# Optimization experiments

Measured on AMD Instinct MI355X. Metric: run time of the kernel, lower is better.

## Reference

```python
import jax, jax.numpy as jnp
import numpy as np

N_NODES = 100000
N_EDGES = 1600000
D_IN = 256
D_OUT = 256


def setup_inputs() -> dict:
    key = jax.random.key(0)
    k1, k2, k3, k4, k5 = jax.random.split(key, 5)
    feat = jax.random.normal(k1, (N_NODES, D_IN), dtype=jnp.float32)
    src = jax.random.randint(k2, (N_EDGES,), 0, N_NODES, dtype=jnp.int32)
    dst = jax.random.randint(k3, (N_EDGES,), 0, N_NODES, dtype=jnp.int32)
    # xavier_uniform with gain for relu (sqrt(2)), as in reset_parameters
    gain = float(np.sqrt(2.0))
    limit = gain * float(np.sqrt(6.0 / (D_IN + D_OUT)))
    w_neigh = jax.random.uniform(k4, (D_OUT, D_IN), minval=-limit, maxval=limit, dtype=jnp.float32)
    w_self = jax.random.uniform(k5, (D_OUT, D_IN), minval=-limit, maxval=limit, dtype=jnp.float32)
    b_self = jnp.zeros((D_OUT,), dtype=jnp.float32)
    return {"feat": feat, "src": src, "dst": dst,
            "w_neigh": w_neigh, "w_self": w_self, "b_self": b_self}


def reference(feat, src, dst, w_neigh, w_self, b_self):
    # SAGEConv, aggregator_type='mean', feat_drop=0, no edge_weight.
    # lin_before_mp = (in_feats > out_feats) = False -> aggregate raw feats first.
    n = feat.shape[0]
    # gather messages at edges and segment-sum into dst nodes
    summed = jax.ops.segment_sum(feat[src], dst, num_segments=n)  # [N, D_in]
    deg = jax.ops.segment_sum(jnp.ones_like(dst, dtype=feat.dtype), dst, num_segments=n)
    h_neigh_raw = summed / jnp.maximum(deg, 1.0)[:, None]  # mean; 0 for isolated nodes
    h_neigh = h_neigh_raw @ w_neigh.T                       # fc_neigh (no bias)
    rst = feat @ w_self.T + b_self + h_neigh                # fc_self(h_self) + h_neigh
    return rst
```

## Files before the change

### kernel.cpp

```cpp
#include <hip/hip_runtime.h>
#include <cstddef>

#define N_NODES 100000
#define N_EDGES 1600000
#define D 256

typedef short          s16x8 __attribute__((ext_vector_type(8)));
typedef unsigned short u16x8 __attribute__((ext_vector_type(8)));
typedef float          f32x4 __attribute__((ext_vector_type(4)));
typedef float          f32x8 __attribute__((ext_vector_type(8)));

__device__ __forceinline__ unsigned short f2bf(float f) {
    unsigned int u = __float_as_uint(f);
    unsigned int r = (u + 0x7fffu + ((u >> 16) & 1u)) >> 16;
    return (unsigned short)r;
}
__device__ __forceinline__ float bf2f(unsigned short u) {
    return __uint_as_float(((unsigned int)u) << 16);
}

#define WS_COUNTS 0
#define WS_ROWPTR (N_NODES)
#define WS_COL    (2 * N_NODES + 16)
#define WS_PART   (WS_COL + N_EDGES)
#define WB_BYTE   ((size_t)(WS_PART + 128) * 4)
#define FB_BYTE   (WB_BYTE + 2 * 65536 * 2)
#define FB_SZ     ((size_t)N_NODES * D * 2)
#define FQ_BYTE   FB_BYTE
#define FQ_SZ     ((size_t)N_NODES * D)
#define HB3_BYTE  (FQ_BYTE + FQ_SZ)
#define NEED_XL3  (HB3_BYTE + FB_SZ)
#define NEED_LARGE (FB_BYTE + FB_SZ)
#define NEED_MID  (FB_BYTE)

#define FBLOCKS (N_NODES * D / 8 / 256)
#define SCAN_NB ((N_NODES + 1023) / 1024)
#define GEMMBLKS ((N_NODES + 63) / 64)
#define NSLICE 8
#define SLICE_N (N_NODES / NSLICE)
#define ECHUNK 2048
#define ECHUNKS ((N_EDGES + ECHUNK - 1) / ECHUNK)
#define SLICED_NB (ECHUNKS * NSLICE)

__global__ __launch_bounds__(256) void cvt_u8_kernel(
    const float* __restrict__ feat, const float* __restrict__ w_self,
    const float* __restrict__ w_neigh,
    unsigned char* __restrict__ fq, unsigned short* __restrict__ wb)
{
    const int b = blockIdx.x;
    if (b < FBLOCKS) {
        const int i = b * 256 + threadIdx.x;
        const f32x8 v = ((const f32x8*)feat)[i];
        unsigned int p0 = 0, p1 = 0;
#pragma unroll
        for (int k = 0; k < 4; ++k) {
            int q = (int)rintf(fminf(fmaxf(v[k] * 16.0f, -127.0f), 127.0f)) + 128;
            p0 |= ((unsigned int)q) << (8 * k);
        }
#pragma unroll
        for (int k = 0; k < 4; ++k) {
            int q = (int)rintf(fminf(fmaxf(v[4 + k] * 16.0f, -127.0f), 127.0f)) + 128;
            p1 |= ((unsigned int)q) << (8 * k);
        }
        uint2 o; o.x = p0; o.y = p1;
        *(uint2*)(fq + (size_t)i * 8) = o;
    } else {
        const int i = (b - FBLOCKS) * 256 + threadIdx.x;
        const bool isself = (i < 16384);
        const float* srcp = isself ? w_self : w_neigh;
        const int j = (isself ? i : i - 16384) * 4;
        const float4 v = *(const float4*)(srcp + j);
        ushort4 o;
        o.x = f2bf(v.x); o.y = f2bf(v.y); o.z = f2bf(v.z); o.w = f2bf(v.w);
        ((ushort4*)wb)[i] = o;
    }
}

__global__ __launch_bounds__(256) void cvt_bf16_kernel(
    const float* __restrict__ feat, const float* __restrict__ w_self,
    const float* __restrict__ w_neigh,
    unsigned short* __restrict__ fb, unsigned short* __restrict__ wb)
{
    const int b = blockIdx.x;
    if (b < FBLOCKS) {
        const int i = b * 256 + threadIdx.x;
        const f32x8 v = ((const f32x8*)feat)[i];
        ushort4 a, c;
        a.x = f2bf(v[0]); a.y = f2bf(v[1]); a.z = f2bf(v[2]); a.w = f2bf(v[3]);
        c.x = f2bf(v[4]); c.y = f2bf(v[5]); c.z = f2bf(v[6]); c.w = f2bf(v[7]);
        ((ushort4*)fb)[i * 2 + 0] = a;
        ((ushort4*)fb)[i * 2 + 1] = c;
    } else {
        const int i = (b - FBLOCKS) * 256 + threadIdx.x;
        const bool isself = (i < 16384);
        const float* srcp = isself ? w_self : w_neigh;
        const int j = (isself ? i : i - 16384) * 4;
        const float4 v = *(const float4*)(srcp + j);
        ushort4 o;
        o.x = f2bf(v.x); o.y = f2bf(v.y); o.z = f2bf(v.z); o.w = f2bf(v.w);
        ((ushort4*)wb)[i] = o;
    }
}

__global__ __launch_bounds__(256) void wcvt_kernel(
    const float* __restrict__ w_self, const float* __restrict__ w_neigh,
    unsigned short* __restrict__ wb)
{
    const int i = blockIdx.x * 256 + threadIdx.x;
    const bool isself = (i < 16384);
    const float* srcp = isself ? w_self : w_neigh;
    const int j = (isself ? i : i - 16384) * 4;
    const float4 v = *(const float4*)(srcp + j);
    ushort4 o;
    o.x = f2bf(v.x); o.y = f2bf(v.y); o.z = f2bf(v.z); o.w = f2bf(v.w);
    ((ushort4*)wb)[i] = o;
}

__global__ __launch_bounds__(256) void hist_sliced_kernel(
    const int* __restrict__ dst, int* __restrict__ counts)
{
    const int slice = blockIdx.x & (NSLICE - 1);
    const int chunk = blockIdx.x >> 3;
    const int lo = slice * SLICE_N, hi = lo + SLICE_N;
    const int e0 = chunk * ECHUNK + threadIdx.x * 8;
    if (e0 >= N_EDGES) return;
    if (e0 + 8 <= N_EDGES) {
        const int4 d0 = *(const int4*)(dst + e0);
        const int4 d1 = *(const int4*)(dst + e0 + 4);
        const int dv[8] = {d0.x, d0.y, d0.z, d0.w, d1.x, d1.y, d1.z, d1.w};
#pragma unroll
        for (int k = 0; k < 8; ++k)
            if (dv[k] >= lo && dv[k] < hi) atomicAdd(&counts[dv[k]], 1);
    } else {
        for (int e = e0; e < N_EDGES; ++e) {
            const int d = dst[e];
            if (d >= lo && d < hi) atomicAdd(&counts[d], 1);
        }
    }
}

__global__ __launch_bounds__(1024) void scan_block_kernel(
    const int* __restrict__ counts, int* __restrict__ row_ptr,
    int* __restrict__ partials)
{
    __shared__ int wsum[16];
    const int t = threadIdx.x, b = blockIdx.x, i = b * 1024 + t;
    const int lane = t & 63, w = t >> 6;
    int x = (i < N_NODES) ? counts[i] : 0;
#pragma unroll
    for (int off = 1; off < 64; off <<= 1) {
        int y = __shfl_up(x, off, 64);
        if (lane >= off) x += y;
    }
    if (lane == 63) wsum[w] = x;
    __syncthreads();
    if (w == 0) {
        int s = (lane < 16) ? wsum[lane] : 0;
#pragma unroll
        for (int off = 1; off < 16; off <<= 1) {
            int y = __shfl_up(s, off, 64);
            if (lane >= off) s += y;
        }
        if (lane < 16) wsum[lane] = s;
    }
    __syncthreads();
    const int incl = x + (w > 0 ? wsum[w - 1] : 0);
    if (i < N_NODES) row_ptr[i + 1] = incl;
    if (t == 1023) partials[b] = incl;
}

__global__ __launch_bounds__(1024) void scan_add2_kernel(
    const int* __restrict__ partials, int* __restrict__ row_ptr)
{
    __shared__ int sp[SCAN_NB];
    const int t = threadIdx.x, b = blockIdx.x;
    if (t < SCAN_NB) sp[t] = partials[t];
    __syncthreads();
    int off = 0;
    for (int j = 0; j < b; ++j) off += sp[j];
    const int i = b * 1024 + t;
    if (i < N_NODES) row_ptr[i + 1] += off;
    if (b == 0 && t == 0) row_ptr[0] = 0;
}

__global__ __launch_bounds__(256) void fill_sliced_kernel(
    const int* __restrict__ src, const int* __restrict__ dst,
    const int* __restrict__ row_ptr, int* __restrict__ counts,
    int* __restrict__ col)
{
    const int slice = blockIdx.x & (NSLICE - 1);
    const int chunk = blockIdx.x >> 3;
    const int lo = slice * SLICE_N, hi = lo + SLICE_N;
    const int e0 = chunk * ECHUNK + threadIdx.x * 8;
    if (e0 >= N_EDGES) return;
    if (e0 + 8 <= N_EDGES) {
        const int4 d0 = *(const int4*)(dst + e0);
        const int4 d1 = *(const int4*)(dst + e0 + 4);
        const int4 s0 = *(const int4*)(src + e0);
        const int4 s1 = *(const int4*)(src + e0 + 4);
        const int dv[8] = {d0.x, d0.y, d0.z, d0.w, d1.x, d1.y, d1.z, d1.w};
        const int sv[8] = {s0.x, s0.y, s0.z, s0.w, s1.x, s1.y, s1.z, s1.w};
#pragma unroll
        for (int k = 0; k < 8; ++k) {
            const int d = dv[k];
            if (d >= lo && d < hi) {
                const int pos = atomicSub(&counts[d], 1) - 1;
                col[row_ptr[d] + pos] = sv[k];
            }
        }
    } else {
        for (int e = e0; e < N_EDGES; ++e) {
            const int d = dst[e];
            if (d >= lo && d < hi) {
                const int pos = atomicSub(&counts[d], 1) - 1;
                col[row_ptr[d] + pos] = src[e];
            }
        }
    }
}

__global__ __launch_bounds__(256) void aggregate4_kernel(
    const unsigned char* __restrict__ fq,
    const int* __restrict__ row_ptr, const int* __restrict__ col,
    unsigned short* __restrict__ hb)
{
    const int node = (blockIdx.x * blockDim.x + threadIdx.x) >> 6;
    const int lane = threadIdx.x & 63;
    if (node >= N_NODES) return;
    const int beg = row_ptr[node], end = row_ptr[node + 1];
    const int quarter = lane >> 4;
    const int chunk = lane & 15;

    unsigned int aE[4] = {0,0,0,0}, aO[4] = {0,0,0,0};
    unsigned int bE[4] = {0,0,0,0}, bO[4] = {0,0,0,0};
    const unsigned char* base = fq + chunk * 16;

    int j = beg + quarter;
    for (; j + 4 < end; j += 8) {
        const int s0 = col[j];
        const int s1 = col[j + 4];
        const uint4 u = *(const uint4*)(base + (size_t)s0 * D);
        const uint4 v = *(const uint4*)(base + (size_t)s1 * D);
        aE[0] += u.x & 0x00FF00FFu;  aO[0] += (u.x >> 8) & 0x00FF00FFu;
        aE[1] += u.y & 0x00FF00FFu;  aO[1] += (u.y >> 8) & 0x00FF00FFu;
        aE[2] += u.z & 0x00FF00FFu;  aO[2] += (u.z >> 8) & 0x00FF00FFu;
        aE[3] += u.w & 0x00FF00FFu;  aO[3] += (u.w >> 8) & 0x00FF00FFu;
        bE[0] += v.x & 0x00FF00FFu;  bO[0] += (v.x >> 8) & 0x00FF00FFu;
        bE[1] += v.y & 0x00FF00FFu;  bO[1] += (v.y >> 8) & 0x00FF00FFu;
        bE[2] += v.z & 0x00FF00FFu;  bO[2] += (v.z >> 8) & 0x00FF00FFu;
        bE[3] += v.w & 0x00FF00FFu;  bO[3] += (v.w >> 8) & 0x00FF00FFu;
    }
    for (; j < end; j += 4) {
        const int s0 = col[j];
        const uint4 u = *(const uint4*)(base + (size_t)s0 * D);
        aE[0] += u.x & 0x00FF00FFu;  aO[0] += (u.x >> 8) & 0x00FF00FFu;
        aE[1] += u.y & 0x00FF00FFu;  aO[1] += (u.y >> 8) & 0x00FF00FFu;
        aE[2] += u.z & 0x00FF00FFu;  aO[2] += (u.z >> 8) & 0x00FF00FFu;
        aE[3] += u.w & 0x00FF00FFu;  aO[3] += (u.w >> 8) & 0x00FF00FFu;
    }

#pragma unroll
    for (int d = 0; d < 4; ++d) {
        unsigned int e = aE[d] + bE[d];
        unsigned int o = aO[d] + bO[d];
        e += __shfl_xor((int)e, 16, 64);
        e += __shfl_xor((int)e, 32, 64);
        o += __shfl_xor((int)o, 16, 64);
        o += __shfl_xor((int)o, 32, 64);
        aE[d] = e; aO[d] = o;
    }

    if (quarter == 0) {
        const int deg = end - beg;
        const float inv = 1.0f / (16.0f * fmaxf((float)deg, 1.0f));
        const float bias = 128.0f * (float)deg;
        u16x8 o0, o1;
#pragma unroll
        for (int d = 0; d < 4; ++d) {
            const float e0 = ((float)(aE[d] & 0xFFFFu) - bias) * inv;
            const float e2 = ((float)(aE[d] >> 16)     - bias) * inv;
            const float e1 = ((float)(aO[d] & 0xFFFFu) - bias) * inv;
            const float e3 = ((float)(aO[d] >> 16)     - bias) * inv;
            if (d < 2) {
                o0[d * 4 + 0] = f2bf(e0); o0[d * 4 + 1] = f2bf(e1);
                o0[d * 4 + 2] = f2bf(e2); o0[d * 4 + 3] = f2bf(e3);
            } else {
                o1[(d - 2) * 4 + 0] = f2bf(e0); o1[(d - 2) * 4 + 1] = f2bf(e1);
                o1[(d - 2) * 4 + 2] = f2bf(e2); o1[(d - 2) * 4 + 3] = f2bf(e3);
            }
        }
        unsigned short* op = hb + (size_t)node * D + chunk * 16;
        *(u16x8*)op = o0;
        *(u16x8*)(op + 8) = o1;
    }
}

__global__ __launch_bounds__(256) void gemm_v5_kernel(
    const float* __restrict__ feat,
    const unsigned short* __restrict__ hb,
    const unsigned short* __restrict__ wb,
    const float* __restrict__ b_self,
    float* __restrict__ outp)
{
    __shared__ unsigned short As[2][64 * 64];

    const int t    = threadIdx.x;
    const int lane = t & 63;
    const int w    = t >> 6;
    const int row0 = blockIdx.x * 64;
    const int c0   = w * 64;
    const int nl   = lane & 15;
    const int kg   = lane >> 4;

    const int tr = t >> 2;
    const int tq = t & 3;
    int grow = row0 + tr; if (grow > N_NODES - 1) grow = N_NODES - 1;
    const size_t gf = (size_t)grow * D;

    int wsw[2];
#pragma unroll
    for (int c = 0; c < 2; ++c) {
        const int cs = tq * 16 + c * 8;
        wsw[c] = tr * 64 + (cs ^ ((tr & 7) << 3));
    }
    int rsw[4][2];
#pragma unroll
    for (int m = 0; m < 4; ++m) {
        const int r = m * 16 + nl;
#pragma unroll
        for (int kk = 0; kk < 2; ++kk) {
            const int cs = kg * 8 + kk * 32;
            rsw[m][kk] = r * 64 + (cs ^ ((r & 7) << 3));
        }
    }

    f32x4 acc[4][4];
#pragma unroll
    for (int m = 0; m < 4; ++m)
#pragma unroll
        for (int n = 0; n < 4; ++n) acc[m][n] = (f32x4){0.f, 0.f, 0.f, 0.f};

    f32x8 fA0, fA1, fB0, fB1;
    u16x8 hA0, hA1, hB0, hB1;

#define LOADSET(F0, F1, H0, H1, S) do {                                       \
        if ((S) < 4) {                                                        \
            F0 = *(const f32x8*)(feat + gf + (S) * 64 + tq * 16);             \
            F1 = *(const f32x8*)(feat + gf + (S) * 64 + tq * 16 + 8);         \
        } else {                                                              \
            H0 = *(const u16x8*)(hb + gf + ((S) & 3) * 64 + tq * 16);         \
            H1 = *(const u16x8*)(hb + gf + ((S) & 3) * 64 + tq * 16 + 8);     \
        }                                                                     \
    } while (0)

#define WRITESET(F0, F1, H0, H1, S) do {                                      \
        u16x8 w0_, w1_;                                                       \
        if ((S) < 4) {                                                        \
            _Pragma("unroll") for (int i_ = 0; i_ < 8; ++i_) {                \
                w0_[i_] = f2bf(F0[i_]); w1_[i_] = f2bf(F1[i_]);               \
            }                                                                 \
        } else { w0_ = H0; w1_ = H1; }                                        \
        *(u16x8*)&As[(S) & 1][wsw[0]] = w0_;                                  \
        *(u16x8*)&As[(S) & 1][wsw[1]] = w1_;                                  \
    } while (0)

    LOADSET(fA0, fA1, hA0, hA1, 0);
    LOADSET(fB0, fB1, hB0, hB1, 1);

#pragma unroll
    for (int s = 0; s < 8; ++s) {
        if ((s & 1) == 0) WRITESET(fA0, fA1, hA0, hA1, s);
        else              WRITESET(fB0, fB1, hB0, hB1, s);
        __syncthreads();
        if (s + 2 < 8) {
            if ((s & 1) == 0) LOADSET(fA0, fA1, hA0, hA1, s + 2);
            else              LOADSET(fB0, fB1, hB0, hB1, s + 2);
        }
        const int hsel = (s < 4) ? 0 : 65536;
        const int kbase = (s & 3) * 64;
#pragma unroll
        for (int kk = 0; kk < 2; ++kk) {
            s16x8 a[4], b[4];
#pragma unroll
            for (int m = 0; m < 4; ++m)
                a[m] = *(const s16x8*)&As[s & 1][rsw[m][kk]];
#pragma unroll
            for (int n = 0; n < 4; ++n)
                b[n] = *(const s16x8*)(wb + hsel
                        + (size_t)(c0 + n * 16 + nl) * 256 + kbase + kk * 32 + kg * 8);
#pragma unroll
            for (int m = 0; m < 4; ++m)
#pragma unroll
                for (int n = 0; n < 4; ++n)
                    acc[m][n] = __builtin_amdgcn_mfma_f32_16x16x32_bf16(
                        a[m], b[n], acc[m][n], 0, 0, 0);
        }
    }
#undef LOADSET
#undef WRITESET

#pragma unroll
    for (int n = 0; n < 4; ++n) {
        const float bias = b_self[c0 + n * 16 + nl];
#pragma unroll
        for (int m = 0; m < 4; ++m) {
            const int rbase = row0 + m * 16 + kg * 4;
#pragma unroll
            for (int r = 0; r < 4; ++r) {
                const int row = rbase + r;
                if (row < N_NODES)
                    outp[(size_t)row * D + c0 + n * 16 + nl] = acc[m][n][r] + bias;
            }
        }
    }
}

__global__ __launch_bounds__(256) void aggregate2f_kernel(
    const unsigned short* __restrict__ featb,
    const int* __restrict__ row_ptr, const int* __restrict__ col,
    float* __restrict__ outf)
{
    const int node = (blockIdx.x * blockDim.x + threadIdx.x) >> 6;
    const int lane = threadIdx.x & 63;
    if (node >= N_NODES) return;
    const int beg = row_ptr[node], end = row_ptr[node + 1];
    const int half = lane >> 5;
    const int chunk = lane & 31;

    float a0[8] = {0,0,0,0,0,0,0,0};
    float a1[8] = {0,0,0,0,0,0,0,0};
    float a2[8] = {0,0,0,0,0,0,0,0};
    float a3[8] = {0,0,0,0,0,0,0,0};
    const unsigned short* fbp = featb + chunk * 8;

    int j = beg + half;
    for (; j + 6 < end; j += 8) {
        const int s0 = col[j], s1 = col[j + 2], s2 = col[j + 4], s3 = col[j + 6];
        const u16x8 u0 = *(const u16x8*)(fbp + (size_t)s0 * D);
        const u16x8 u1 = *(const u16x8*)(fbp + (size_t)s1 * D);
        const u16x8 u2 = *(const u16x8*)(fbp + (size_t)s2 * D);
        const u16x8 u3 = *(const u16x8*)(fbp + (size_t)s3 * D);
#pragma unroll
        for (int i = 0; i < 8; ++i) a0[i] += bf2f(u0[i]);
#pragma unroll
        for (int i = 0; i < 8; ++i) a1[i] += bf2f(u1[i]);
#pragma unroll
        for (int i = 0; i < 8; ++i) a2[i] += bf2f(u2[i]);
#pragma unroll
        for (int i = 0; i < 8; ++i) a3[i] += bf2f(u3[i]);
    }
    for (; j < end; j += 2) {
        const int s0 = col[j];
        const u16x8 u0 = *(const u16x8*)(fbp + (size_t)s0 * D);
#pragma unroll
        for (int i = 0; i < 8; ++i) a0[i] += bf2f(u0[i]);
    }

    const float invd = 1.0f / fmaxf((float)(end - beg), 1.0f);
    float tv[8];
#pragma unroll
    for (int i = 0; i < 8; ++i) {
        float v = (a0[i] + a1[i]) + (a2[i] + a3[i]);
        v += __shfl_xor(v, 32, 64);
        tv[i] = v * invd;
    }
    float4 o;
    o.x = tv[half * 4 + 0]; o.y = tv[half * 4 + 1];
    o.z = tv[half * 4 + 2]; o.w = tv[half * 4 + 3];
    *(float4*)(outf + (size_t)node * D + chunk * 8 + half * 4) = o;
}

__global__ __launch_bounds__(256) void aggregate_f32_kernel(
    const float* __restrict__ feat, const int* __restrict__ row_ptr,
    const int* __restrict__ col, float* __restrict__ outf)
{
    const int node = (blockIdx.x * blockDim.x + threadIdx.x) >> 6;
    const int lane = threadIdx.x & 63;
    if (node >= N_NODES) return;
    const int beg = row_ptr[node], end = row_ptr[node + 1];

    float4 a0 = make_float4(0.f, 0.f, 0.f, 0.f);
    float4 a1 = make_float4(0.f, 0.f, 0.f, 0.f);
    float4 a2 = make_float4(0.f, 0.f, 0.f, 0.f);
    float4 a3 = make_float4(0.f, 0.f, 0.f, 0.f);

#define ACC(acc, s)                                                          \
    do {                                                                     \
        const float4 v = ((const float4*)(feat + (size_t)(s) * D))[lane];    \
        acc.x += v.x; acc.y += v.y; acc.z += v.z; acc.w += v.w;              \
    } while (0)

    int j = beg;
    for (; j + 3 < end; j += 4) {
        const int s0 = col[j], s1 = col[j + 1], s2 = col[j + 2], s3 = col[j + 3];
        ACC(a0, s0); ACC(a1, s1); ACC(a2, s2); ACC(a3, s3);
    }
    for (; j < end; ++j) { const int s0 = col[j]; ACC(a0, s0); }
#undef ACC

    const float invd = 1.0f / fmaxf((float)(end - beg), 1.0f);
    float4 r;
    r.x = ((a0.x + a1.x) + (a2.x + a3.x)) * invd;
    r.y = ((a0.y + a1.y) + (a2.y + a3.y)) * invd;
    r.z = ((a0.z + a1.z) + (a2.z + a3.z)) * invd;
    r.w = ((a0.w + a1.w) + (a2.w + a3.w)) * invd;
    ((float4*)(outf + (size_t)node * D))[lane] = r;
}

__global__ __launch_bounds__(256) void gemm_mfma64_f32h_kernel(
    const float* __restrict__ feat,
    const unsigned short* __restrict__ wb,
    const float* __restrict__ b_self,
    const float* h32, float* outp)
{
    const int lane = threadIdx.x & 63;
    const int wslice = threadIdx.x >> 6;
    const int row0 = blockIdx.x * 64;
    const int c0 = wslice * 64;
    const int nl = lane & 15;
    const int kg = lane >> 4;

    f32x4 acc[4][4];
#pragma unroll
    for (int m = 0; m < 4; ++m)
#pragma unroll
        for (int n = 0; n < 4; ++n) acc[m][n] = (f32x4){0.f, 0.f, 0.f, 0.f};

    size_t aoff[4];
#pragma unroll
    for (int m = 0; m < 4; ++m) {
        int r = row0 + m * 16 + nl;
        if (r > N_NODES - 1) r = N_NODES - 1;
        aoff[m] = (size_t)r * D + kg * 8;
    }

#pragma unroll
    for (int hf = 0; hf < 2; ++hf) {
        const unsigned short* wh = wb + hf * 65536 + (size_t)(c0 + nl) * 256 + kg * 8;
#pragma unroll
        for (int kk = 0; kk < 8; ++kk) {
            const int kb = kk * 32;
            s16x8 afrag[4];
#pragma unroll
            for (int m = 0; m < 4; ++m) {
                const float* ap = hf == 0 ? (const float*)feat : h32;
                const f32x8 av = *(const f32x8*)(ap + aoff[m] + kb);
#pragma unroll
                for (int i = 0; i < 8; ++i) afrag[m][i] = (short)f2bf(av[i]);
            }
            s16x8 bfrag[4];
#pragma unroll
            for (int n = 0; n < 4; ++n)
                bfrag[n] = *(const s16x8*)(wh + n * 4096 + kb);
#pragma unroll
            for (int m = 0; m < 4; ++m)
#pragma unroll
                for (int n = 0; n < 4; ++n)
                    acc[m][n] = __builtin_amdgcn_mfma_f32_16x16x32_bf16(
                        afrag[m], bfrag[n], acc[m][n], 0, 0, 0);
        }
    }

    __syncthreads();

#pragma unroll
    for (int n = 0; n < 4; ++n) {
        const float bias = b_self[c0 + n * 16 + nl];
#pragma unroll
        for (int m = 0; m < 4; ++m) {
            const int rbase = row0 + m * 16 + kg * 4;
#pragma unroll
            for (int r = 0; r < 4; ++r) {
                const int row = rbase + r;
                if (row < N_NODES)
                    outp[(size_t)row * D + c0 + n * 16 + nl] = acc[m][n][r] + bias;
            }
        }
    }
}

__global__ __launch_bounds__(256) void scatter_kernel(
    const float* __restrict__ feat, const int* __restrict__ src,
    const int* __restrict__ dst, float* __restrict__ S, float* __restrict__ deg)
{
    const int gtid = blockIdx.x * blockDim.x + threadIdx.x;
    const int wave = gtid >> 6;
    const int lane = gtid & 63;
    const int nwaves = (gridDim.x * blockDim.x) >> 6;
    for (int e = wave; e < N_EDGES; e += nwaves) {
        const int s = src[e];
        const int d = dst[e];
        if (lane == 0) unsafeAtomicAdd(&deg[d], 1.0f);
        const float4 v = ((const float4*)(feat + (size_t)s * D))[lane];
        float* o = S + (size_t)d * D + lane * 4;
        unsafeAtomicAdd(o + 0, v.x);
        unsafeAtomicAdd(o + 1, v.y);
        unsafeAtomicAdd(o + 2, v.z);
        unsafeAtomicAdd(o + 3, v.w);
    }
}

#define BM 64
#define BK 16

__global__ __launch_bounds__(256) void fused_gemm_f32(
    const float* __restrict__ feat, const float* __restrict__ w_neigh,
    const float* __restrict__ w_self, const float* __restrict__ b_self,
    const float* __restrict__ deg, float* out)
{
    __shared__ float At[BK][BM + 4];
    __shared__ float Bt[BK][256];

    const int tid = threadIdx.x;
    const int i0 = blockIdx.x * BM;
    const int trow = tid >> 4;
    const int tcol = tid & 15;
    const int m_load = tid >> 2;
    const int kq = tid & 3;

    const int arow = i0 + m_load;
    const bool arow_ok = arow < N_NODES;
    float invd = 1.0f;
    if (arow_ok) invd = 1.0f / fmaxf(deg[arow], 1.0f);

    float acc[4][16];
#pragma unroll
    for (int r = 0; r < 4; ++r)
#pragma unroll
        for (int c = 0; c < 16; ++c) acc[r][c] = 0.0f;

    for (int kc = 0; kc < (2 * D) / BK; ++kc) {
        const int kb = kc * BK;
        const bool self_part = (kb < D);
        const int kbase = self_part ? kb : (kb - D);

        float4 va = make_float4(0.f, 0.f, 0.f, 0.f);
        if (arow_ok) {
            const float* ap = self_part ? feat : out;
            va = *(const float4*)(ap + (size_t)arow * D + kbase + kq * 4);
            if (!self_part) { va.x *= invd; va.y *= invd; va.z *= invd; va.w *= invd; }
        }
        const float* W = self_part ? w_self : w_neigh;
        const float4* wp = (const float4*)(W + (size_t)tid * D + kbase);
        const float4 w0 = wp[0], w1 = wp[1], w2 = wp[2], w3 = wp[3];

        __syncthreads();
        At[kq * 4 + 0][m_load] = va.x;
        At[kq * 4 + 1][m_load] = va.y;
        At[kq * 4 + 2][m_load] = va.z;
        At[kq * 4 + 3][m_load] = va.w;
        Bt[ 0][tid] = w0.x; Bt[ 1][tid] = w0.y; Bt[ 2][tid] = w0.z; Bt[ 3][tid] = w0.w;
        Bt[ 4][tid] = w1.x; Bt[ 5][tid] = w1.y; Bt[ 6][tid] = w1.z; Bt[ 7][tid] = w1.w;
        Bt[ 8][tid] = w2.x; Bt[ 9][tid] = w2.y; Bt[10][tid] = w2.z; Bt[11][tid] = w2.w;
        Bt[12][tid] = w3.x; Bt[13][tid] = w3.y; Bt[14][tid] = w3.z; Bt[15][tid] = w3.w;
        __syncthreads();

#pragma unroll
        for (int k = 0; k < BK; ++k) {
            const float4 a = *(const float4*)&At[k][trow * 4];
            float4 b[4];
#pragma unroll
            for (int g = 0; g < 4; ++g)
                b[g] = *(const float4*)&Bt[k][g * 64 + tcol * 4];
            const float av[4] = {a.x, a.y, a.z, a.w};
#pragma unroll
            for (int r = 0; r < 4; ++r)
#pragma unroll
                for (int g = 0; g < 4; ++g) {
                    acc[r][g * 4 + 0] = fmaf(av[r], b[g].x, acc[r][g * 4 + 0]);
                    acc[r][g * 4 + 1] = fmaf(av[r], b[g].y, acc[r][g * 4 + 1]);
                    acc[r][g * 4 + 2] = fmaf(av[r], b[g].z, acc[r][g * 4 + 2]);
                    acc[r][g * 4 + 3] = fmaf(av[r], b[g].w, acc[r][g * 4 + 3]);
                }
        }
    }

    float4 bias[4];
#pragma unroll
    for (int g = 0; g < 4; ++g)
        bias[g] = *(const float4*)&b_self[g * 64 + tcol * 4];

#pragma unroll
    for (int r = 0; r < 4; ++r) {
        const int row = i0 + trow * 4 + r;
        if (row < N_NODES) {
            float* op = out + (size_t)row * D;
#pragma unroll
            for (int g = 0; g < 4; ++g) {
                float4 v;
                v.x = acc[r][g * 4 + 0] + bias[g].x;
                v.y = acc[r][g * 4 + 1] + bias[g].y;
                v.z = acc[r][g * 4 + 2] + bias[g].z;
                v.w = acc[r][g * 4 + 3] + bias[g].w;
                *(float4*)(op + g * 64 + tcol * 4) = v;
            }
        }
    }
}

extern "C" void kernel_launch(void* const* d_in, const int* in_sizes, int n_in,
                              void* d_out, int out_size, void* d_ws, size_t ws_size,
                              hipStream_t stream) {
    const float* feat    = (const float*)d_in[0];
    const int*   src     = (const int*)d_in[1];
    const int*   dst     = (const int*)d_in[2];
    const float* w_neigh = (const float*)d_in[3];
    const float* w_self  = (const float*)d_in[4];
    const float* b_self  = (const float*)d_in[5];
    float* out = (float*)d_out;

    const int ablocks = (N_NODES * 64 + 255) / 256;

    if (ws_size >= NEED_MID) {
        int* wsI     = (int*)d_ws;
        int* counts  = wsI + WS_COUNTS;
        int* row_ptr = wsI + WS_ROWPTR;
        int* col     = wsI + WS_COL;
        int* part    = wsI + WS_PART;
        unsigned short* wb = (unsigned short*)((char*)d_ws + WB_BYTE);
        unsigned short* fb = (unsigned short*)((char*)d_ws + FB_BYTE);
        unsigned char*  fq = (unsigned char*)((char*)d_ws + FQ_BYTE);
        unsigned short* hb = (unsigned short*)((char*)d_ws + HB3_BYTE);

        hipMemsetAsync(counts, 0, N_NODES * sizeof(int), stream);
        if (ws_size >= NEED_XL3)
            cvt_u8_kernel<<<FBLOCKS + 128, 256, 0, stream>>>(
                feat, w_self, w_neigh, fq, wb);
        else if (ws_size >= NEED_LARGE)
            cvt_bf16_kernel<<<FBLOCKS + 128, 256, 0, stream>>>(
                feat, w_self, w_neigh, fb, wb);
        else
            wcvt_kernel<<<128, 256, 0, stream>>>(w_self, w_neigh, wb);

        hist_sliced_kernel<<<SLICED_NB, 256, 0, stream>>>(dst, counts);
        scan_block_kernel<<<SCAN_NB, 1024, 0, stream>>>(counts, row_ptr, part);
        scan_add2_kernel<<<SCAN_NB, 1024, 0, stream>>>(part, row_ptr);
        fill_sliced_kernel<<<SLICED_NB, 256, 0, stream>>>(
            src, dst, row_ptr, counts, col);

        if (ws_size >= NEED_XL3) {
            aggregate4_kernel<<<ablocks, 256, 0, stream>>>(fq, row_ptr, col, hb);
            gemm_v5_kernel<<<GEMMBLKS, 256, 0, stream>>>(feat, hb, wb, b_self, out);
        } else if (ws_size >= NEED_LARGE) {
            aggregate2f_kernel<<<ablocks, 256, 0, stream>>>(
                fb, row_ptr, col, out);
            gemm_mfma64_f32h_kernel<<<GEMMBLKS, 256, 0, stream>>>(
                feat, wb, b_self, out, out);
        } else {
            aggregate_f32_kernel<<<ablocks, 256, 0, stream>>>(
                feat, row_ptr, col, out);
            gemm_mfma64_f32h_kernel<<<GEMMBLKS, 256, 0, stream>>>(
                feat, wb, b_self, out, out);
        }
    } else {
        float* deg = (float*)d_ws;
        hipMemsetAsync(out, 0, (size_t)N_NODES * D * sizeof(float), stream);
        hipMemsetAsync(deg, 0, (size_t)N_NODES * sizeof(float), stream);
        scatter_kernel<<<4096, 256, 0, stream>>>(feat, src, dst, out, deg);
        fused_gemm_f32<<<(N_NODES + BM - 1) / BM, 256, 0, stream>>>(
            feat, w_neigh, w_self, b_self, deg, out);
    }
}
```

Baseline: 348.8 us.

## Slice quantized features by column and aggregate per slice for cache locality

The u8 quantized feature table is stored as 8 column slices of 32 bytes per node instead of row-major 256 bytes. The aggregation kernel now assigns each block to one slice, with 32 lanes per node each gathering 16 bytes from 16 edges in parallel, then reduces by shuffles. The aim is to keep each slice's 3.2 MB working set resident in L2/MALL during random gathers, at the cost of 8x more edge-list reads and more shuffle reductions.

```diff
diff --git a/kernel.cpp b/kernel.cpp
--- a/kernel.cpp
+++ b/kernel.cpp
@@ -28,6 +28,7 @@
 #define FB_SZ     ((size_t)N_NODES * D * 2)
 #define FQ_BYTE   FB_BYTE
 #define FQ_SZ     ((size_t)N_NODES * D)
+#define SLICE_B   ((size_t)N_NODES * 32)
 #define HB3_BYTE  (FQ_BYTE + FQ_SZ)
 #define NEED_XL3  (HB3_BYTE + FB_SZ)
 #define NEED_LARGE (FB_BYTE + FB_SZ)
@@ -41,6 +42,7 @@
 #define ECHUNK 2048
 #define ECHUNKS ((N_EDGES + ECHUNK - 1) / ECHUNK)
 #define SLICED_NB (ECHUNKS * NSLICE)
+#define A5_NB ((N_NODES + 7) / 8 * 8)
 
 __global__ __launch_bounds__(256) void cvt_u8_kernel(
     const float* __restrict__ feat, const float* __restrict__ w_self,
@@ -50,7 +52,9 @@
     const int b = blockIdx.x;
     if (b < FBLOCKS) {
         const int i = b * 256 + threadIdx.x;
-        const f32x8 v = ((const f32x8*)feat)[i];
+        const int n = i >> 5;
+        const int c0 = (i & 31) * 8;
+        const f32x8 v = *(const f32x8*)(feat + (size_t)n * D + c0);
         unsigned int p0 = 0, p1 = 0;
 #pragma unroll
         for (int k = 0; k < 4; ++k) {
@@ -63,7 +67,7 @@
             p1 |= ((unsigned int)q) << (8 * k);
         }
         uint2 o; o.x = p0; o.y = p1;
-        *(uint2*)(fq + (size_t)i * 8) = o;
+        *(uint2*)(fq + (size_t)(c0 >> 5) * SLICE_B + (size_t)n * 32 + (c0 & 31)) = o;
     } else {
         const int i = (b - FBLOCKS) * 256 + threadIdx.x;
         const bool isself = (i < 16384);
@@ -219,58 +223,51 @@
     }
 }
 
-__global__ __launch_bounds__(256) void aggregate4_kernel(
+__global__ __launch_bounds__(256) void aggregate5_kernel(
     const unsigned char* __restrict__ fq,
     const int* __restrict__ row_ptr, const int* __restrict__ col,
     unsigned short* __restrict__ hb)
 {
-    const int node = (blockIdx.x * blockDim.x + threadIdx.x) >> 6;
-    const int lane = threadIdx.x & 63;
+    const int slice = blockIdx.x & 7;
+    const int group = blockIdx.x >> 3;
+    const int wid   = threadIdx.x >> 6;
+    const int lane  = threadIdx.x & 63;
+    const int sub   = lane >> 5;
+    const int l     = lane & 31;
+    const int e     = l >> 1;
+    const int c     = l & 1;
+
+    const int node = group * 8 + wid * 2 + sub;
     if (node >= N_NODES) return;
     const int beg = row_ptr[node], end = row_ptr[node + 1];
-    const int quarter = lane >> 4;
-    const int chunk = lane & 15;
+
+    const unsigned char* base = fq + (size_t)slice * SLICE_B + c * 16;
 
     unsigned int aE[4] = {0,0,0,0}, aO[4] = {0,0,0,0};
-    unsigned int bE[4] = {0,0,0,0}, bO[4] = {0,0,0,0};
-    const unsigned char* base = fq + chunk * 16;
-
-    int j = beg + quarter;
-    for (; j + 4 < end; j += 8) {
+    for (int j = beg + e; j < end; j += 16) {
         const int s0 = col[j];
-        const int s1 = col[j + 4];
-        const uint4 u = *(const uint4*)(base + (size_t)s0 * D);
-        const uint4 v = *(const uint4*)(base + (size_t)s1 * D);
+        const uint4 u = *(const uint4*)(base + (size_t)s0 * 32);
         aE[0] += u.x & 0x00FF00FFu;  aO[0] += (u.x >> 8) & 0x00FF00FFu;
         aE[1] += u.y & 0x00FF00FFu;  aO[1] += (u.y >> 8) & 0x00FF00FFu;
         aE[2] += u.z & 0x00FF00FFu;  aO[2] += (u.z >> 8) & 0x00FF00FFu;
         aE[3] += u.w & 0x00FF00FFu;  aO[3] += (u.w >> 8) & 0x00FF00FFu;
-        bE[0] += v.x & 0x00FF00FFu;  bO[0] += (v.x >> 8) & 0x00FF00FFu;
-        bE[1] += v.y & 0x00FF00FFu;  bO[1] += (v.y >> 8) & 0x00FF00FFu;
-        bE[2] += v.z & 0x00FF00FFu;  bO[2] += (v.z >> 8) & 0x00FF00FFu;
-        bE[3] += v.w & 0x00FF00FFu;  bO[3] += (v.w >> 8) & 0x00FF00FFu;
-    }
-    for (; j < end; j += 4) {
-        const int s0 = col[j];
-        const uint4 u = *(const uint4*)(base + (size_t)s0 * D);
-        aE[0] += u.x & 0x00FF00FFu;  aO[0] += (u.x >> 8) & 0x00FF00FFu;
-        aE[1] += u.y & 0x00FF00FFu;  aO[1] += (u.y >> 8) & 0x00FF00FFu;
-        aE[2] += u.z & 0x00FF00FFu;  aO[2] += (u.z >> 8) & 0x00FF00FFu;
-        aE[3] += u.w & 0x00FF00FFu;  aO[3] += (u.w >> 8) & 0x00FF00FFu;
     }
 
 #pragma unroll
     for (int d = 0; d < 4; ++d) {
-        unsigned int e = aE[d] + bE[d];
-        unsigned int o = aO[d] + bO[d];
-        e += __shfl_xor((int)e, 16, 64);
-        e += __shfl_xor((int)e, 32, 64);
-        o += __shfl_xor((int)o, 16, 64);
-        o += __shfl_xor((int)o, 32, 64);
-        aE[d] = e; aO[d] = o;
-    }
-
-    if (quarter == 0) {
+        unsigned int ev = aE[d], ov = aO[d];
+        ev += __shfl_xor((int)ev, 2, 64);
+        ev += __shfl_xor((int)ev, 4, 64);
+        ev += __shfl_xor((int)ev, 8, 64);
+        ev += __shfl_xor((int)ev, 16, 64);
+        ov += __shfl_xor((int)ov, 2, 64);
+        ov += __shfl_xor((int)ov, 4, 64);
+        ov += __shfl_xor((int)ov, 8, 64);
+        ov += __shfl_xor((int)ov, 16, 64);
+        aE[d] = ev; aO[d] = ov;
+    }
+
+    if (e == 0) {
         const int deg = end - beg;
         const float inv = 1.0f / (16.0f * fmaxf((float)deg, 1.0f));
         const float bias = 128.0f * (float)deg;
@@ -289,7 +286,7 @@
                 o1[(d - 2) * 4 + 2] = f2bf(e2); o1[(d - 2) * 4 + 3] = f2bf(e3);
             }
         }
-        unsigned short* op = hb + (size_t)node * D + chunk * 16;
+        unsigned short* op = hb + (size_t)node * D + slice * 32 + c * 16;
         *(u16x8*)op = o0;
         *(u16x8*)(op + 8) = o1;
     }
@@ -739,7 +736,7 @@
             src, dst, row_ptr, counts, col);
 
         if (ws_size >= NEED_XL3) {
-            aggregate4_kernel<<<ablocks, 256, 0, stream>>>(fq, row_ptr, col, hb);
+            aggregate5_kernel<<<A5_NB, 256, 0, stream>>>(fq, row_ptr, col, hb);
             gemm_v5_kernel<<<GEMMBLKS, 256, 0, stream>>>(feat, hb, wb, b_self, out);
         } else if (ws_size >= NEED_LARGE) {
             aggregate2f_kernel<<<ablocks, 256, 0, stream>>>(
```

Result: slower. 412.5 us (+18.3%).
